# Performance work log

Measured on AMD Instinct MI355X. Metric: run time of the kernel, lower is better.

Reference implementation:

```python
import jax, jax.numpy as jnp
import numpy as np

B, T, F = 64, 1024, 4
INF = jnp.float32(1e30)


def _dtw_cost(p, q):
    """Accumulated DTW cost matrix. p: [T1,2], q: [T2,2]. Returns C: [T1,T2].

    Recurrence C[i,j] = D[i,j] + min(C[i-1,j], C[i,j-1], C[i-1,j-1]).
    The within-row dependency c_j = d_j + min(a_j, c_{j-1}) (with
    a_j = min(C[i-1,j], C[i-1,j-1])) is a min-plus scan, solved in closed
    form: c_j = S_j + cummin_k<=j (a_k - S_{k-1}), S = cumsum(d).
    """
    # pairwise Euclidean distance (dtw.dtw2d uses 2D Euclidean)
    D = jnp.sqrt(jnp.sum((p[:, None, :] - q[None, :, :]) ** 2, axis=-1))  # [T1,T2]

    c0 = jnp.cumsum(D[0])  # first row: only left moves allowed

    def row(prev, d):
        shifted = jnp.concatenate([jnp.full((1,), INF, prev.dtype), prev[:-1]])
        a = jnp.minimum(prev, shifted)          # min(C[i-1,j], C[i-1,j-1])
        S = jnp.cumsum(d)
        Sprev = jnp.concatenate([jnp.zeros((1,), d.dtype), S[:-1]])
        m = jax.lax.associative_scan(jnp.minimum, a - Sprev)
        c = S + m
        return c, c

    _, rest = jax.lax.scan(row, c0, D[1:])
    return jnp.concatenate([c0[None, :], rest], axis=0)


def _dtw_path(C):
    """Backtrace alignment path from C. Returns (a, b, valid) each [T1+T2-1]."""
    T1, T2 = C.shape
    L = T1 + T2 - 1

    def step(carry, _):
        i, j, done = carry
        at0 = (i == 0) & (j == 0)
        cd = jnp.where((i > 0) & (j > 0), C[i - 1, j - 1], INF)
        cu = jnp.where(i > 0, C[i - 1, j], INF)
        cl = jnp.where(j > 0, C[i, j - 1], INF)
        k = jnp.argmin(jnp.stack([cd, cu, cl]))  # diag preferred on ties
        di = jnp.where(k == 2, 0, 1)
        dj = jnp.where(k == 1, 0, 1)
        ni = jnp.where(at0, 0, i - di)
        nj = jnp.where(at0, 0, j - dj)
        return (ni, nj, done | at0), (i, j, jnp.logical_not(done))

    init = (jnp.int32(T1 - 1), jnp.int32(T2 - 1), jnp.bool_(False))
    _, (a, b, valid) = jax.lax.scan(step, init, None, length=L)
    return a, b, valid


def _single_loss(pred, targ, subcoef):
    # DTW alignment computed on (x, y) basis, detached (torch runs it in numpy)
    p = jax.lax.stop_gradient(pred[:, :2])
    q = jax.lax.stop_gradient(targ[:, :2])
    C = _dtw_cost(p, q)
    a, b, valid = _dtw_path(C)
    # gather aligned points on loss_indices = [0, 1], L1 loss weighted by subcoef
    pg = pred[a, :2]  # [L, 2]
    tg = targ[b, :2]
    w = valid[:, None].astype(pred.dtype)
    return jnp.sum(jnp.abs(pg - tg) * subcoef[None, :] * w)


def setup_inputs() -> dict:
    key = jax.random.key(0)
    k1, k2 = jax.random.split(key)
    preds = jax.random.normal(k1, (B, T, F), dtype=jnp.float32)
    targs = jax.random.normal(k2, (B, T, F), dtype=jnp.float32)
    subcoef = jnp.ones((2,), dtype=jnp.float32)
    return {"preds": preds, "targs": targs, "subcoef": subcoef}


def reference(preds, targs, subcoef):
    losses = jax.vmap(lambda p, t: _single_loss(p, t, subcoef))(preds, targs)
    return jnp.sum(losses)
```

## Files before the change

kernel.cpp:

```cpp
#include <hip/hip_runtime.h>

#define TT   1024
#define NW   34
#define NPH  (NW + 9)
#define FINF 1e30f

template<bool A> struct BoolC { static constexpr bool value = A; };


__device__ __forceinline__ float dpp_wave_shr1(float x) {
    return __int_as_float(__builtin_amdgcn_update_dpp(
        0, __float_as_int(x), 0x138, 0xF, 0xF, false));
}

__global__ __launch_bounds__(256) void dtw_forward(
    const float* __restrict__ preds,
    const float* __restrict__ targs,
    uint2* __restrict__ dirs)
{
    __shared__ float2 qsh[TT];
    __shared__ float  mbox[3][TT];

    const int tid  = threadIdx.x;
    const int w    = tid >> 6;
    const int lane = tid & 63;
    const int b    = blockIdx.x;

    for (int k = tid; k < TT; k += 256) {
        float4 t4 = ((const float4*)targs)[(size_t)b * TT + k];
        qsh[k] = make_float2(t4.x, t4.y);
    }
    for (int k = tid; k < 3 * TT; k += 256) ((float*)mbox)[k] = FINF;

    float px[4], py[4];
    {
        const int row0 = w * 256 + 4 * lane;
#pragma unroll
        for (int r = 0; r < 4; ++r) {
            float4 pv = ((const float4*)preds)[(size_t)b * TT + row0 + r];
            px[r] = pv.x; py[r] = pv.y;
        }
    }
    __syncthreads();

    const float* src = (w > 0) ? mbox[w - 1] : nullptr;
    float*       dst = (w < 3) ? mbox[w]     : nullptr;

    float cur0 = FINF, cur1 = FINF, cur2 = FINF, cur3 = FINF;
    float uprev = FINF, shp = FINF;
    unsigned au0 = 0, ad0 = 0, au1 = 0, ad1 = 0;
    unsigned au2 = 0, ad2 = 0, au3 = 0, ad3 = 0;
    float bnd[8];
#pragma unroll
    for (int k = 0; k < 8; ++k) bnd[k] = FINF;

    const int bi  = 4 * w + (lane >> 4);
    const int rr0 = 4 * (lane & 15);
    const bool is63 = (lane == 63);

    for (int G = 0; G < NPH; ++G) {
        const int T = G - 3 * w;
        if ((unsigned)T < (unsigned)NW) {
            auto body = [&](auto actc) {
                constexpr bool ACT = decltype(actc)::value;
#pragma unroll 1
                for (int sub = 0; sub < 4; ++sub) {
                    const int s0 = 32 * T + 8 * sub;
                    float qx[8], qy[8];
#pragma unroll
                    for (int k2 = 0; k2 < 8; ++k2) {
                        float2 qv = qsh[(s0 + k2 - lane) & (TT - 1)];
                        qx[k2] = qv.x; qy[k2] = qv.y;
                    }
                    if (w > 0 && s0 < TT) {
#pragma unroll
                        for (int k2 = 0; k2 < 8; ++k2) bnd[k2] = src[s0 + k2];
                    }
                    float bq[8];
#pragma unroll
                    for (int k2 = 0; k2 < 8; ++k2) {
                        const int s = s0 + k2;
                        float d[4];
#pragma unroll
                        for (int r = 0; r < 4; ++r) {
                            const float dx = px[r] - qx[k2];
                            const float dy = py[r] - qy[k2];
                            d[r] = __builtin_amdgcn_sqrtf(dx * dx + dy * dy);
                        }

                        const float u = (lane == 0) ? ((w == 0) ? FINF : bnd[k2]) : shp;
                        const float c0o = cur0, c1o = cur1, c2o = cur2, c3o = cur3;

                        float m2a = fminf(u, c0o);
                        float ba  = fminf(uprev, m2a);
                        if constexpr (ACT) ba = (ba > 9e29f) ? 0.0f : ba;
                        const float v0 = d[0] + ba;
                        const unsigned bd0 = (uprev <= m2a) ? 1u : 0u;
                        const unsigned bu0 = ((u <= c0o) ? 1u : 0u) | bd0;
                        float m2b = fminf(v0, c1o);
                        const float v1 = d[1] + fminf(c0o, m2b);
                        const unsigned bd1 = (c0o <= m2b) ? 1u : 0u;
                        const unsigned bu1 = ((v0 <= c1o) ? 1u : 0u) | bd1;
                        float m2c = fminf(v1, c2o);
                        const float v2 = d[2] + fminf(c1o, m2c);
                        const unsigned bd2 = (c1o <= m2c) ? 1u : 0u;
                        const unsigned bu2 = ((v1 <= c2o) ? 1u : 0u) | bd2;
                        float m2d = fminf(v2, c3o);
                        const float v3 = d[3] + fminf(c2o, m2d);
                        const unsigned bd3 = (c2o <= m2d) ? 1u : 0u;
                        const unsigned bu3 = ((v2 <= c3o) ? 1u : 0u) | bd3;

                        au0 = (au0 << 1) | bu0;  ad0 = (ad0 << 1) | bd0;
                        au1 = (au1 << 1) | bu1;  ad1 = (ad1 << 1) | bd1;
                        au2 = (au2 << 1) | bu2;  ad2 = (ad2 << 1) | bd2;
                        au3 = (au3 << 1) | bu3;  ad3 = (ad3 << 1) | bd3;

                        if constexpr (ACT) {
                            const bool act = (lane <= s);
                            cur0 = act ? v0 : c0o;
                            cur1 = act ? v1 : c1o;
                            cur2 = act ? v2 : c2o;
                            cur3 = act ? v3 : c3o;
                        } else {
                            cur0 = v0; cur1 = v1; cur2 = v2; cur3 = v3;
                        }
                        uprev = u;
                        bq[k2] = cur3;
                        shp = dpp_wave_shr1(cur3);
                    }
                    if (is63 && w < 3) {
#pragma unroll
                        for (int k2 = 0; k2 < 8; ++k2) {
                            const int c = s0 + k2 - 63;
                            if ((unsigned)c < 1024u) dst[c] = bq[k2];
                        }
                    }
                }
            };
            if (T < 2) body(BoolC<true>{}); else body(BoolC<false>{});

            const size_t base = (size_t)((b * 16 + bi) * NW + T) * 64 + rr0;
            uint4* dp = (uint4*)&dirs[base];
            dp[0] = make_uint4(__builtin_bitreverse32(au0), __builtin_bitreverse32(ad0),
                               __builtin_bitreverse32(au1), __builtin_bitreverse32(ad1));
            dp[1] = make_uint4(__builtin_bitreverse32(au2), __builtin_bitreverse32(ad2),
                               __builtin_bitreverse32(au3), __builtin_bitreverse32(ad3));
            au0 = ad0 = au1 = ad1 = au2 = ad2 = au3 = ad3 = 0u;
        }
        __syncthreads();
    }
}

__global__ __launch_bounds__(1024) void dtw_exits(
    const uint2* __restrict__ dirs,
    unsigned short* __restrict__ exitc)
{
    __shared__ uint2 raw[NW * 64];
    __shared__ unsigned nebit[64][32];
    __shared__ unsigned dgbit[64][32];

    const int tid = threadIdx.x;
    const int b = blockIdx.x >> 4, bi = blockIdx.x & 15;

    for (int i = tid; i < NW * 64; i += 1024)
        raw[i] = dirs[(size_t)(b * 16 + bi) * (NW * 64) + i];
    __syncthreads();
    for (int i = tid; i < 64 * 32; i += 1024) {
        const int rr = i >> 5, u = i & 31;
        const int o  = ((bi & 3) << 4) + (rr >> 2);
        const int T0 = u + (o >> 5), sh = o & 31;
        uint2 A  = raw[T0 * 64 + rr];
        uint2 Bv = raw[(T0 + 1) * 64 + rr];
        nebit[rr][u] = sh ? ((A.x >> sh) | (Bv.x << (32 - sh))) : A.x;
        dgbit[rr][u] = sh ? ((A.y >> sh) | (Bv.y << (32 - sh))) : A.y;
    }
    __syncthreads();

    int j = tid;
    for (int rr = 63; rr >= 0; --rr) {
        if (bi == 0 && rr == 0) { j = 0; break; }
        int u = j >> 5, m = j & 31;
        unsigned wv = nebit[rr][u] << (31 - m);
        while (wv == 0u && u > 0) { --u; wv = nebit[rr][u]; m = 31; }
        const int j2 = (wv == 0u) ? 0 : ((u << 5) + m - __builtin_clz(wv));
        const int diag = (int)((dgbit[rr][j2 >> 5] >> (j2 & 31)) & 1u);
        j = j2 - diag;
        if (j < 0) j = 0;
    }
    exitc[((size_t)(b * 16 + bi) << 10) + tid] = (unsigned short)j;
}

__global__ void dtw_entries(const unsigned short* __restrict__ exitc,
                            unsigned short* __restrict__ ent)
{
    const int b = threadIdx.x;
    int j = TT - 1;
    for (int bi = 15; bi >= 0; --bi) {
        ent[b * 16 + bi] = (unsigned short)j;
        j = exitc[((size_t)(b * 16 + bi) << 10) + j];
    }
}

__global__ __launch_bounds__(64) void dtw_loss(
    const float* __restrict__ preds,
    const float* __restrict__ targs,
    const float* __restrict__ subcoef,
    const uint2* __restrict__ dirs,
    const unsigned short* __restrict__ ent,
    float* __restrict__ out)
{
    __shared__ uint2 raw[NW * 64];
    __shared__ unsigned nebit[64][32];
    __shared__ unsigned dgbit[64][32];
    __shared__ float2 qsh[TT];
    __shared__ float2 psh[64];
    __shared__ unsigned recs[160];

    const int lane = threadIdx.x;
    const int b = blockIdx.x >> 4, bi = blockIdx.x & 15;

    for (int i = lane; i < NW * 64; i += 64)
        raw[i] = dirs[(size_t)(b * 16 + bi) * (NW * 64) + i];
    for (int k = lane; k < TT; k += 64) {
        float4 t4 = ((const float4*)targs)[(size_t)b * TT + k];
        qsh[k] = make_float2(t4.x, t4.y);
    }
    {
        float4 p4 = ((const float4*)preds)[(size_t)b * TT + bi * 64 + lane];
        psh[lane] = make_float2(p4.x, p4.y);
    }
    __syncthreads();
    for (int i = lane; i < 64 * 32; i += 64) {
        const int rr = i >> 5, u = i & 31;
        const int o  = ((bi & 3) << 4) + (rr >> 2);
        const int T0 = u + (o >> 5), sh = o & 31;
        uint2 A  = raw[T0 * 64 + rr];
        uint2 Bv = raw[(T0 + 1) * 64 + rr];
        nebit[rr][u] = sh ? ((A.x >> sh) | (Bv.x << (32 - sh))) : A.x;
        dgbit[rr][u] = sh ? ((A.y >> sh) | (Bv.y << (32 - sh))) : A.y;
    }
    __syncthreads();

    int j = ent[b * 16 + bi];
    int nrec = 0;
    for (int rr = 63; rr >= 0; --rr) {
        int j2;
        if (bi == 0 && rr == 0) j2 = 0;
        else {
            int u = j >> 5, m = j & 31;
            unsigned wv = nebit[rr][u] << (31 - m);
            while (wv == 0u && u > 0) { --u; wv = nebit[rr][u]; m = 31; }
            j2 = (wv == 0u) ? 0 : ((u << 5) + m - __builtin_clz(wv));
        }
        int c = j;
        for (;;) {
            int cl = (c - 31 > j2) ? (c - 31) : j2;
            if (lane == 0)
                recs[nrec] = ((unsigned)rr << 20) | ((unsigned)cl << 10) | (unsigned)c;
            ++nrec;
            if (cl == j2) break;
            c = cl - 1;
        }
        if (bi == 0 && rr == 0) j = 0;
        else {
            const int diag = (int)((dgbit[rr][j2 >> 5] >> (j2 & 31)) & 1u);
            j = j2 - diag;
            if (j < 0) j = 0;
        }
    }
    __syncthreads();

    const float sc0 = subcoef[0], sc1 = subcoef[1];
    float acc = 0.0f;
    for (int k = lane; k < nrec; k += 64) {
        unsigned rec = recs[k];
        int rr = (int)(rec >> 20), cl = (int)((rec >> 10) & 1023u), ch = (int)(rec & 1023u);
        float2 p = psh[rr];
        for (int c = cl; c <= ch; ++c) {
            float2 q = qsh[c];
            acc += fabsf(p.x - q.x) * sc0 + fabsf(p.y - q.y) * sc1;
        }
    }
    for (int o = 32; o; o >>= 1) acc += __shfl_down(acc, o);
    if (lane == 0) atomicAdd(out, acc);
}

extern "C" void kernel_launch(void* const* d_in, const int* in_sizes, int n_in,
                              void* d_out, int out_size, void* d_ws, size_t ws_size,
                              hipStream_t stream)
{
    const float* preds   = (const float*)d_in[0];
    const float* targs   = (const float*)d_in[1];
    const float* subcoef = (const float*)d_in[2];
    float* out = (float*)d_out;

    const int B = in_sizes[0] / (TT * 4);

    const size_t dirsBytes = (size_t)B * 16 * NW * 64 * sizeof(uint2);
    const size_t exitBytes = (size_t)B * 16 * 1024 * sizeof(unsigned short);
    uint2* dirs = (uint2*)d_ws;
    unsigned short* exitc = (unsigned short*)((char*)d_ws + dirsBytes);
    unsigned short* ent   = (unsigned short*)((char*)d_ws + dirsBytes + exitBytes);

    hipMemsetAsync(out, 0, sizeof(float), stream);
    dtw_forward<<<dim3(B), dim3(256), 0, stream>>>(preds, targs, dirs);
    dtw_exits<<<dim3(B * 16), dim3(1024), 0, stream>>>(dirs, exitc);
    dtw_entries<<<dim3(1), dim3(B), 0, stream>>>(exitc, ent);
    dtw_loss<<<dim3(B * 16), dim3(64), 0, stream>>>(preds, targs, subcoef, dirs, ent, out);
}
```

Measured before the change: 411.9 us.

## Split DTW forward wavefront across eight waves with two rows per lane

The forward DTW kernel now uses 8 waves per batch (512 threads), each lane owning 2 rows instead of 4. The per-step serial dependency chain per lane gets shorter while the pipeline gains more stages (NPH grows to NW+21). The kernel also prefetches the next sub-block's q values and boundary values into registers, and folds the lane-0 boundary injection into the DPP old-value operand. The direction-bit layout and the offset math in the exits and loss kernels are adjusted to match. In exchange it adds more pipeline fill/drain phases, more __syncthreads rounds, and higher register pressure from prefetching.

Measured after the change: 425.5 us. +3.3%, slower.

```diff
diff --git a/kernel.cpp b/kernel.cpp
--- a/kernel.cpp
+++ b/kernel.cpp
@@ -2,139 +2,139 @@
 
 #define TT   1024
 #define NW   34
-#define NPH  (NW + 9)
+#define NPH  (NW + 21)
 #define FINF 1e30f
 
 template<bool A> struct BoolC { static constexpr bool value = A; };
 
 
-__device__ __forceinline__ float dpp_wave_shr1(float x) {
+__device__ __forceinline__ float dpp_shr1_old(float oldv, float x) {
     return __int_as_float(__builtin_amdgcn_update_dpp(
-        0, __float_as_int(x), 0x138, 0xF, 0xF, false));
-}
-
-__global__ __launch_bounds__(256) void dtw_forward(
+        __float_as_int(oldv), __float_as_int(x), 0x138, 0xF, 0xF, false));
+}
+
+__global__ __launch_bounds__(512) void dtw_forward(
     const float* __restrict__ preds,
     const float* __restrict__ targs,
     uint2* __restrict__ dirs)
 {
     __shared__ float2 qsh[TT];
-    __shared__ float  mbox[3][TT];
+    __shared__ float  mbox[7][TT];
 
     const int tid  = threadIdx.x;
     const int w    = tid >> 6;
     const int lane = tid & 63;
     const int b    = blockIdx.x;
 
-    for (int k = tid; k < TT; k += 256) {
+    for (int k = tid; k < TT; k += 512) {
         float4 t4 = ((const float4*)targs)[(size_t)b * TT + k];
         qsh[k] = make_float2(t4.x, t4.y);
     }
-    for (int k = tid; k < 3 * TT; k += 256) ((float*)mbox)[k] = FINF;
-
-    float px[4], py[4];
+    for (int k = tid; k < 7 * TT; k += 512) ((float*)mbox)[k] = FINF;
+
+    float px0, py0, px1, py1;
     {
-        const int row0 = w * 256 + 4 * lane;
-#pragma unroll
-        for (int r = 0; r < 4; ++r) {
-            float4 pv = ((const float4*)preds)[(size_t)b * TT + row0 + r];
-            px[r] = pv.x; py[r] = pv.y;
-        }
+        const int row0 = w * 128 + 2 * lane;
+        float4 pv = ((const float4*)preds)[(size_t)b * TT + row0];
+        px0 = pv.x; py0 = pv.y;
+        float4 pw = ((const float4*)preds)[(size_t)b * TT + row0 + 1];
+        px1 = pw.x; py1 = pw.y;
     }
     __syncthreads();
 
     const float* src = (w > 0) ? mbox[w - 1] : nullptr;
-    float*       dst = (w < 3) ? mbox[w]     : nullptr;
-
-    float cur0 = FINF, cur1 = FINF, cur2 = FINF, cur3 = FINF;
-    float uprev = FINF, shp = FINF;
+    float*       dst = (w < 7) ? mbox[w]     : nullptr;
+
+    float cur0 = FINF, cur1 = FINF, uprev = FINF, ucur = FINF;
     unsigned au0 = 0, ad0 = 0, au1 = 0, ad1 = 0;
-    unsigned au2 = 0, ad2 = 0, au3 = 0, ad3 = 0;
-    float bnd[8];
-#pragma unroll
-    for (int k = 0; k < 8; ++k) bnd[k] = FINF;
-
-    const int bi  = 4 * w + (lane >> 4);
-    const int rr0 = 4 * (lane & 15);
+
+    const int bi  = 2 * w + (lane >> 5);
+    const int rr0 = 2 * (lane & 31);
     const bool is63 = (lane == 63);
 
     for (int G = 0; G < NPH; ++G) {
         const int T = G - 3 * w;
         if ((unsigned)T < (unsigned)NW) {
+            float bndc[8];
+#pragma unroll
+            for (int k = 0; k < 8; ++k) bndc[k] = FINF;
+            if (w > 0 && 32 * T < TT) {
+#pragma unroll
+                for (int k = 0; k < 8; ++k) bndc[k] = src[32 * T + k];
+            }
+            if (T == 0) ucur = bndc[0];
+            float2 qc[8];
+#pragma unroll
+            for (int k = 0; k < 8; ++k)
+                qc[k] = qsh[(32 * T + k - lane) & (TT - 1)];
             auto body = [&](auto actc) {
                 constexpr bool ACT = decltype(actc)::value;
 #pragma unroll 1
                 for (int sub = 0; sub < 4; ++sub) {
                     const int s0 = 32 * T + 8 * sub;
-                    float qx[8], qy[8];
-#pragma unroll
-                    for (int k2 = 0; k2 < 8; ++k2) {
-                        float2 qv = qsh[(s0 + k2 - lane) & (TT - 1)];
-                        qx[k2] = qv.x; qy[k2] = qv.y;
-                    }
-                    if (w > 0 && s0 < TT) {
-#pragma unroll
-                        for (int k2 = 0; k2 < 8; ++k2) bnd[k2] = src[s0 + k2];
+                    float bndn[8];
+                    float2 qn[8];
+                    float bndx = FINF;
+#pragma unroll
+                    for (int k = 0; k < 8; ++k) bndn[k] = FINF;
+                    if (sub < 3) {
+                        if (w > 0 && s0 + 8 < TT) {
+#pragma unroll
+                            for (int k = 0; k < 8; ++k) bndn[k] = src[s0 + 8 + k];
+                        }
+#pragma unroll
+                        for (int k = 0; k < 8; ++k)
+                            qn[k] = qsh[(s0 + 8 + k - lane) & (TT - 1)];
+                    } else {
+                        if (w > 0 && s0 + 8 < TT) bndx = src[s0 + 8];
                     }
                     float bq[8];
 #pragma unroll
                     for (int k2 = 0; k2 < 8; ++k2) {
                         const int s = s0 + k2;
-                        float d[4];
-#pragma unroll
-                        for (int r = 0; r < 4; ++r) {
-                            const float dx = px[r] - qx[k2];
-                            const float dy = py[r] - qy[k2];
-                            d[r] = __builtin_amdgcn_sqrtf(dx * dx + dy * dy);
-                        }
-
-                        const float u = (lane == 0) ? ((w == 0) ? FINF : bnd[k2]) : shp;
-                        const float c0o = cur0, c1o = cur1, c2o = cur2, c3o = cur3;
-
-                        float m2a = fminf(u, c0o);
-                        float ba  = fminf(uprev, m2a);
-                        if constexpr (ACT) ba = (ba > 9e29f) ? 0.0f : ba;
-                        const float v0 = d[0] + ba;
-                        const unsigned bd0 = (uprev <= m2a) ? 1u : 0u;
-                        const unsigned bu0 = ((u <= c0o) ? 1u : 0u) | bd0;
-                        float m2b = fminf(v0, c1o);
-                        const float v1 = d[1] + fminf(c0o, m2b);
-                        const unsigned bd1 = (c0o <= m2b) ? 1u : 0u;
-                        const unsigned bu1 = ((v0 <= c1o) ? 1u : 0u) | bd1;
-                        float m2c = fminf(v1, c2o);
-                        const float v2 = d[2] + fminf(c1o, m2c);
-                        const unsigned bd2 = (c1o <= m2c) ? 1u : 0u;
-                        const unsigned bu2 = ((v1 <= c2o) ? 1u : 0u) | bd2;
-                        float m2d = fminf(v2, c3o);
-                        const float v3 = d[3] + fminf(c2o, m2d);
-                        const unsigned bd3 = (c2o <= m2d) ? 1u : 0u;
-                        const unsigned bu3 = ((v2 <= c3o) ? 1u : 0u) | bd3;
+                        const float dx0 = px0 - qc[k2].x, dy0 = py0 - qc[k2].y;
+                        const float d0 = __builtin_amdgcn_sqrtf(dx0 * dx0 + dy0 * dy0);
+                        const float dx1 = px1 - qc[k2].x, dy1 = py1 - qc[k2].y;
+                        const float d1 = __builtin_amdgcn_sqrtf(dx1 * dx1 + dy1 * dy1);
+
+                        const float u = ucur;
+                        float ba0 = fminf(fminf(u, cur0), uprev);
+                        const unsigned bd0 = (uprev == ba0) ? 1u : 0u;
+                        const unsigned bu0 = ((u <= cur0) ? 1u : 0u) | bd0;
+                        if constexpr (ACT) ba0 = (ba0 > 9e29f) ? 0.0f : ba0;
+                        const float v0 = d0 + ba0;
+                        const float ba1 = fminf(fminf(v0, cur1), cur0);
+                        const unsigned bd1 = (cur0 == ba1) ? 1u : 0u;
+                        const unsigned bu1 = ((v0 <= cur1) ? 1u : 0u) | bd1;
+                        const float v1 = d1 + ba1;
 
                         au0 = (au0 << 1) | bu0;  ad0 = (ad0 << 1) | bd0;
                         au1 = (au1 << 1) | bu1;  ad1 = (ad1 << 1) | bd1;
-                        au2 = (au2 << 1) | bu2;  ad2 = (ad2 << 1) | bd2;
-                        au3 = (au3 << 1) | bu3;  ad3 = (ad3 << 1) | bd3;
 
                         if constexpr (ACT) {
                             const bool act = (lane <= s);
-                            cur0 = act ? v0 : c0o;
-                            cur1 = act ? v1 : c1o;
-                            cur2 = act ? v2 : c2o;
-                            cur3 = act ? v3 : c3o;
+                            cur0 = act ? v0 : cur0;
+                            cur1 = act ? v1 : cur1;
                         } else {
-                            cur0 = v0; cur1 = v1; cur2 = v2; cur3 = v3;
+                            cur0 = v0; cur1 = v1;
                         }
                         uprev = u;
-                        bq[k2] = cur3;
-                        shp = dpp_wave_shr1(cur3);
+                        bq[k2] = cur1;
+                        const float oldv = (k2 < 7) ? bndc[k2 + 1]
+                                         : ((sub < 3) ? bndn[0] : bndx);
+                        ucur = dpp_shr1_old(oldv, cur1);
                     }
-                    if (is63 && w < 3) {
+                    if (is63 && w < 7) {
 #pragma unroll
                         for (int k2 = 0; k2 < 8; ++k2) {
                             const int c = s0 + k2 - 63;
                             if ((unsigned)c < 1024u) dst[c] = bq[k2];
                         }
                     }
+                    if (sub < 3) {
+#pragma unroll
+                        for (int k = 0; k < 8; ++k) { qc[k] = qn[k]; bndc[k] = bndn[k]; }
+                    }
                 }
             };
             if (T < 2) body(BoolC<true>{}); else body(BoolC<false>{});
@@ -143,9 +143,7 @@
             uint4* dp = (uint4*)&dirs[base];
             dp[0] = make_uint4(__builtin_bitreverse32(au0), __builtin_bitreverse32(ad0),
                                __builtin_bitreverse32(au1), __builtin_bitreverse32(ad1));
-            dp[1] = make_uint4(__builtin_bitreverse32(au2), __builtin_bitreverse32(ad2),
-                               __builtin_bitreverse32(au3), __builtin_bitreverse32(ad3));
-            au0 = ad0 = au1 = ad1 = au2 = ad2 = au3 = ad3 = 0u;
+            au0 = ad0 = au1 = ad1 = 0u;
         }
         __syncthreads();
     }
@@ -167,7 +165,7 @@
     __syncthreads();
     for (int i = tid; i < 64 * 32; i += 1024) {
         const int rr = i >> 5, u = i & 31;
-        const int o  = ((bi & 3) << 4) + (rr >> 2);
+        const int o  = ((bi & 1) << 5) + (rr >> 1);
         const int T0 = u + (o >> 5), sh = o & 31;
         uint2 A  = raw[T0 * 64 + rr];
         uint2 Bv = raw[(T0 + 1) * 64 + rr];
@@ -232,7 +230,7 @@
     __syncthreads();
     for (int i = lane; i < 64 * 32; i += 64) {
         const int rr = i >> 5, u = i & 31;
-        const int o  = ((bi & 3) << 4) + (rr >> 2);
+        const int o  = ((bi & 1) << 5) + (rr >> 1);
         const int T0 = u + (o >> 5), sh = o & 31;
         uint2 A  = raw[T0 * 64 + rr];
         uint2 Bv = raw[(T0 + 1) * 64 + rr];
@@ -303,7 +301,7 @@
     unsigned short* ent   = (unsigned short*)((char*)d_ws + dirsBytes + exitBytes);
 
     hipMemsetAsync(out, 0, sizeof(float), stream);
-    dtw_forward<<<dim3(B), dim3(256), 0, stream>>>(preds, targs, dirs);
+    dtw_forward<<<dim3(B), dim3(512), 0, stream>>>(preds, targs, dirs);
     dtw_exits<<<dim3(B * 16), dim3(1024), 0, stream>>>(dirs, exitc);
     dtw_entries<<<dim3(1), dim3(B), 0, stream>>>(exitc, ent);
     dtw_loss<<<dim3(B * 16), dim3(64), 0, stream>>>(preds, targs, subcoef, dirs, ent, out);
```
